# Kernel optimization log

Measured on AMD Instinct MI355X. Metric: run time of the kernel, lower is better.

Reference implementation:

```python
import jax, jax.numpy as jnp
import numpy as np

N_EMBED = 512  # scaling uses n_embed**-0.5 (as in the original, not head_dim)

def setup_inputs() -> dict:
    key = jax.random.key(0)
    k1, k2, k3 = jax.random.split(key, 3)
    B, T, HD = 4, 4096, 64
    return {
        "k": jax.random.normal(k1, (B, T, HD), dtype=jnp.float32),
        "q": jax.random.normal(k2, (B, T, HD), dtype=jnp.float32),
        "v": jax.random.normal(k3, (B, T, HD), dtype=jnp.float32),
    }

def reference(k, q, v):
    # wei = q @ k^T * n_embed^-0.5  -> [B, T, T]
    scale = N_EMBED ** (-0.5)
    wei = jnp.einsum("bqd,bkd->bqk", q, k) * scale
    T = q.shape[1]
    causal = jnp.tril(jnp.ones((T, T), dtype=bool))  # [T, T]
    wei = jnp.where(causal, wei, -jnp.inf)
    wei = jax.nn.softmax(wei, axis=-1)
    # dropout p=0.0 (identity)
    out = jnp.einsum("bqk,bkd->bqd", wei, v)
    return out
```

## Files before the change

### kernel.cpp

```cpp
#include <hip/hip_runtime.h>
#include <hip/hip_bf16.h>
#include <math.h>


typedef __attribute__((ext_vector_type(8))) __bf16 bf16x8;
typedef __attribute__((ext_vector_type(8))) short  short8;
typedef __attribute__((ext_vector_type(4))) float  f32x4;

#define TT 4096
#define DD 64
#define CH 6
#define NCHUNK_PB 187
#define NSLOT (NCHUNK_PB * 4)

static constexpr float SCALE_L2E = 0.06375871665087779f;

__device__ __forceinline__ ushort f2bf(float x) {
    return __builtin_bit_cast(ushort, (__bf16)x);
}
__device__ __forceinline__ float bf2f(ushort u) {
    return __builtin_bit_cast(float, ((unsigned)u) << 16);
}

__global__ __launch_bounds__(256, 1)
void prep(const float* __restrict__ K, const float* __restrict__ V,
          ushort* __restrict__ Kbf, ushort* __restrict__ Vtbf) {
    const int bx = blockIdx.x;
    const int b = bx & 3, kt = bx >> 2;
    const size_t tbase = (size_t)bx * 4096;
    const size_t gbase = (size_t)b * TT * DD + (size_t)(kt << 6) * DD;
    const int tid = threadIdx.x;

    {
        const int row = tid >> 2, q4 = tid & 3;
        const float* src = K + gbase + row * 64 + q4 * 16;
        ushort* dst = Kbf + tbase + row * 64;
        #pragma unroll
        for (int h = 0; h < 2; ++h) {
            f32x4 x = *(const f32x4*)(src + h * 8);
            f32x4 y = *(const f32x4*)(src + h * 8 + 4);
            union { ushort u[8]; short8 s; } pk;
            #pragma unroll
            for (int j = 0; j < 4; ++j) {
                pk.u[j]     = f2bf(x[j]);
                pk.u[j + 4] = f2bf(y[j]);
            }
            const int ch = (q4 * 2 + h) ^ (row & 7);
            *(short8*)(dst + ch * 8) = pk.s;
        }
    }
    {
        const int kp = tid & 31, dg = tid >> 5;
        const float* v0 = V + gbase + dg * 8 + kp * 2 * 64;
        f32x4 a0 = *(const f32x4*)(v0);
        f32x4 a1 = *(const f32x4*)(v0 + 4);
        f32x4 b0 = *(const f32x4*)(v0 + 64);
        f32x4 b1 = *(const f32x4*)(v0 + 68);
        #pragma unroll
        for (int j = 0; j < 8; ++j) {
            float xa = (j < 4) ? a0[j & 3] : a1[j & 3];
            float xb = (j < 4) ? b0[j & 3] : b1[j & 3];
            unsigned pk2 = (unsigned)f2bf(xa) | ((unsigned)f2bf(xb) << 16);
            const int dim = dg * 8 + j;
            const int off = dim * 64 + (((kp >> 2) ^ j) << 3) + ((kp * 2) & 7);
            *(unsigned*)(Vtbf + tbase + off) = pk2;
        }
    }
}

__global__ __launch_bounds__(256, 3)
void attn_part(const ushort* __restrict__ Kbf, const float* __restrict__ Q,
               const ushort* __restrict__ Vtbf,
               ushort* __restrict__ Opart, float* __restrict__ Lpart) {
    const int bx = blockIdx.x;
    const int b  = bx & 3;
    const int chunkid = bx >> 2;
    int s = 0, base = 0;
    for (;;) {
        const int nch = (s + 3) / 3;
        if (chunkid < base + nch) break;
        base += nch; ++s;
    }
    const int chunk = chunkid - base;

    const int tid = threadIdx.x;
    const int w = tid >> 6, lane = tid & 63;
    const int g = lane >> 4, c = lane & 15;
    const int qw0 = (s << 7) + (w << 5);

    __shared__ ushort lKV[2][2][4096];
    __shared__ ushort lP [4][1024];

    const int kt0 = chunk * CH;
    const int nst = min(kt0 + CH, 2 * (s + 1)) - kt0;
    const int seg0 = w * 1024;
    const int loff = lane * 8;

    {
        const size_t tb = (size_t)((kt0 << 2) | b) * 4096;
        #pragma unroll
        for (int p = 0; p < 2; ++p) {
            const int seg = seg0 + p * 512;
            __builtin_amdgcn_global_load_lds(
                (const __attribute__((address_space(1))) void*)(Kbf + tb + seg + loff),
                (__attribute__((address_space(3))) void*)&lKV[0][0][seg], 16, 0, 0);
            __builtin_amdgcn_global_load_lds(
                (const __attribute__((address_space(1))) void*)(Vtbf + tb + seg + loff),
                (__attribute__((address_space(3))) void*)&lKV[0][1][seg], 16, 0, 0);
        }
    }

    bf16x8 qf[2][2];
    #pragma unroll
    for (int m = 0; m < 2; ++m) {
        const float* qp = Q + (size_t)b * TT * DD
                        + (size_t)(qw0 + m * 16 + c) * DD + g * 8;
        #pragma unroll
        for (int ks = 0; ks < 2; ++ks) {
            f32x4 a = *(const f32x4*)(qp + ks * 32);
            f32x4 d = *(const f32x4*)(qp + ks * 32 + 4);
            bf16x8 t;
            #pragma unroll
            for (int j = 0; j < 4; ++j) {
                t[j]     = (__bf16)(a[j] * SCALE_L2E);
                t[j + 4] = (__bf16)(d[j] * SCALE_L2E);
            }
            qf[m][ks] = t;
        }
    }

    f32x4 acc[2][4];
    #pragma unroll
    for (int m = 0; m < 2; ++m)
        #pragma unroll
        for (int nt = 0; nt < 4; ++nt) acc[m][nt] = (f32x4){0.f, 0.f, 0.f, 0.f};
    float l_p[2][4] = {{0.f,0.f,0.f,0.f},{0.f,0.f,0.f,0.f}};

    for (int st = 0; st < nst; ++st) {
        const int kt = kt0 + st;
        const int kb = kt << 6;
        const int cur = st & 1;

        __syncthreads();

        if (st + 1 < nst) {
            const size_t tb = (size_t)(((kt + 1) << 2) | b) * 4096;
            #pragma unroll
            for (int p = 0; p < 2; ++p) {
                const int seg = seg0 + p * 512;
                __builtin_amdgcn_global_load_lds(
                    (const __attribute__((address_space(1))) void*)(Kbf + tb + seg + loff),
                    (__attribute__((address_space(3))) void*)&lKV[cur ^ 1][0][seg], 16, 0, 0);
                __builtin_amdgcn_global_load_lds(
                    (const __attribute__((address_space(1))) void*)(Vtbf + tb + seg + loff),
                    (__attribute__((address_space(3))) void*)&lKV[cur ^ 1][1][seg], 16, 0, 0);
            }
        }

        if (kb > qw0 + 31) continue;
        const bool act0 = (kb <= qw0 + 15);

        const ushort* lK  = lKV[cur][0];
        const ushort* lVt = lKV[cur][1];

        f32x4 S[2][4];
        #pragma unroll
        for (int nt = 0; nt < 4; ++nt) {
            const int row = nt * 16 + c;
            bf16x8 kf0 = __builtin_bit_cast(bf16x8,
                *(const short8*)&lK[row * 64 + (((0 * 4 + g) ^ (c & 7)) << 3)]);
            bf16x8 kf1 = __builtin_bit_cast(bf16x8,
                *(const short8*)&lK[row * 64 + (((1 * 4 + g) ^ (c & 7)) << 3)]);
            #pragma unroll
            for (int m = 0; m < 2; ++m) {
                if (m == 0 && !act0) continue;
                f32x4 sm = (f32x4){0.f, 0.f, 0.f, 0.f};
                sm = __builtin_amdgcn_mfma_f32_16x16x32_bf16(qf[m][0], kf0, sm, 0, 0, 0);
                sm = __builtin_amdgcn_mfma_f32_16x16x32_bf16(qf[m][1], kf1, sm, 0, 0, 0);
                S[m][nt] = sm;
            }
        }

        bf16x8 pf[2][2];
        #pragma unroll
        for (int m = 0; m < 2; ++m) {
            if (m == 0 && !act0) continue;
            const int qm0 = qw0 + m * 16;
            if (kb + 63 > qm0) {
                #pragma unroll
                for (int nt = 0; nt < 4; ++nt)
                    #pragma unroll
                    for (int r = 0; r < 4; ++r)
                        if (kb + nt * 16 + c > qm0 + g * 4 + r) S[m][nt][r] = -INFINITY;
            }
            ushort* myP = lP[w];
            #pragma unroll
            for (int nt = 0; nt < 4; ++nt)
                #pragma unroll
                for (int r = 0; r < 4; ++r) {
                    const float P = exp2f(S[m][nt][r]);
                    l_p[m][r] += P;
                    const int row = g * 4 + r;
                    const int col = nt * 16 + c;
                    myP[row * 64 + (((col >> 3) ^ (row & 7)) << 3) + (col & 7)] =
                        f2bf(P);
                }
            #pragma unroll
            for (int ks = 0; ks < 2; ++ks)
                pf[m][ks] = __builtin_bit_cast(bf16x8,
                    *(const short8*)&myP[c * 64 + (((ks * 4 + g) ^ (c & 7)) << 3)]);
        }

        #pragma unroll
        for (int ks = 0; ks < 2; ++ks)
            #pragma unroll
            for (int nt = 0; nt < 4; ++nt) {
                bf16x8 vf = __builtin_bit_cast(bf16x8,
                    *(const short8*)&lVt[(nt * 16 + c) * 64 + (((ks * 4 + g) ^ (c & 7)) << 3)]);
                #pragma unroll
                for (int m = 0; m < 2; ++m) {
                    if (m == 0 && !act0) continue;
                    acc[m][nt] = __builtin_amdgcn_mfma_f32_16x16x32_bf16(
                        pf[m][ks], vf, acc[m][nt], 0, 0, 0);
                }
            }
    }

    const int slot = bx;
    #pragma unroll
    for (int m = 0; m < 2; ++m) {
        #pragma unroll
        for (int r = 0; r < 4; ++r) {
            float l = l_p[m][r];
            #pragma unroll
            for (int off = 8; off >= 1; off >>= 1)
                l += __shfl_xor(l, off);
            l_p[m][r] = l;
        }
        union { ushort u[16]; short8 s8[2]; } pk;
        #pragma unroll
        for (int nt = 0; nt < 4; ++nt)
            #pragma unroll
            for (int r = 0; r < 4; ++r)
                pk.u[nt * 4 + r] = f2bf(acc[m][nt][r]);
        ushort* op = Opart + (size_t)slot * 8192 + (w * 2 + m) * 1024 + lane * 16;
        *(short8*)op       = pk.s8[0];
        *(short8*)(op + 8) = pk.s8[1];
        if (c == 0) {
            #pragma unroll
            for (int r = 0; r < 4; ++r)
                Lpart[(size_t)slot * 128 + (w * 2 + m) * 16 + g * 4 + r] = l_p[m][r];
        }
    }
}

__global__ __launch_bounds__(256, 1)
void attn_merge(const ushort* __restrict__ Opart, const float* __restrict__ Lpart,
                float* __restrict__ Out) {
    const int bx = blockIdx.x;
    const int b = bx & 3, s = (bx >> 2) & 31, w = bx >> 7;
    const int tid = threadIdx.x;
    const int m = tid >> 7, half = (tid >> 6) & 1, lane = tid & 63;
    const int g = lane >> 4;
    const int c = lane & 15;
    int base = 0;
    for (int t = 0; t < s; ++t) base += (t + 3) / 3;
    const int nch = (s + 3) / 3;

    float v[8];
    #pragma unroll
    for (int i = 0; i < 8; ++i) v[i] = 0.f;
    f32x4 lsum = (f32x4){0.f, 0.f, 0.f, 0.f};

    for (int ci = 0; ci < nch; ++ci) {
        const int slot = ((base + ci) << 2) | b;
        const ushort* op = Opart + (size_t)slot * 8192
                         + (w * 2 + m) * 1024 + lane * 16 + half * 8;
        short8 sv = *(const short8*)op;
        #pragma unroll
        for (int i = 0; i < 8; ++i) v[i] += bf2f((ushort)sv[i]);
        f32x4 lv = *(const f32x4*)(Lpart + (size_t)slot * 128 + (w * 2 + m) * 16 + g * 4);
        #pragma unroll
        for (int r = 0; r < 4; ++r) lsum[r] += lv[r];
    }

    f32x4 inv;
    #pragma unroll
    for (int r = 0; r < 4; ++r) inv[r] = 1.0f / lsum[r];

    const int qbase = (s << 7) + (w * 2 + m) * 16 + g * 4;
    float* dst = Out + (size_t)b * TT * DD;
    #pragma unroll
    for (int i = 0; i < 8; ++i) {
        const int nt = half * 2 + (i >> 2), r = i & 3;
        dst[(size_t)(qbase + r) * DD + nt * 16 + c] = v[i] * inv[r];
    }
}

__global__ __launch_bounds__(256, 1)
void attn_head(const float* __restrict__ K, const float* __restrict__ Q,
               const float* __restrict__ V, float* __restrict__ Out) {
    const int bx = blockIdx.x;
    const int b  = bx & 3;
    const int qt = bx >> 2;
    const int qbase = qt << 6;
    const int tid = threadIdx.x;
    const int w = tid >> 6, lane = tid & 63;
    const int g = lane >> 4, c = lane & 15;
    const int qr0 = qbase + (w << 4);

    __shared__ ushort lK [64 * 64];
    __shared__ ushort lVt[64 * 64];
    __shared__ ushort lP [4][16 * 64];

    const size_t bbase = (size_t)b * TT * DD;
    bf16x8 qf[2];
    {
        const float* qp = Q + bbase + (size_t)(qr0 + c) * DD + g * 8;
        #pragma unroll
        for (int ks = 0; ks < 2; ++ks) {
            f32x4 a = *(const f32x4*)(qp + ks * 32);
            f32x4 d = *(const f32x4*)(qp + ks * 32 + 4);
            bf16x8 t;
            #pragma unroll
            for (int j = 0; j < 4; ++j) {
                t[j]     = (__bf16)(a[j] * SCALE_L2E);
                t[j + 4] = (__bf16)(d[j] * SCALE_L2E);
            }
            qf[ks] = t;
        }
    }
    f32x4 acc[4];
    #pragma unroll
    for (int nt = 0; nt < 4; ++nt) acc[nt] = (f32x4){0.f, 0.f, 0.f, 0.f};
    float l_r[4] = {0.f, 0.f, 0.f, 0.f};
    const int e0  = w * 1024 + lane * 8;
    const int kch = ((lane & 7) ^ ((lane >> 3) & 7)) << 3;
    const int kp  = tid & 31, dg = tid >> 5;
    const int nkt = qt + 1;
    for (int kt = 0; kt < nkt; ++kt) {
        const int kb = kt << 6;
        __syncthreads();
        {
            const float* src = K + bbase + (size_t)kb * DD;
            #pragma unroll
            for (int p = 0; p < 2; ++p) {
                const int e = e0 + p * 512;
                f32x4 x = *(const f32x4*)(src + e);
                f32x4 y = *(const f32x4*)(src + e + 4);
                union { ushort u[8]; short8 s; } pk;
                #pragma unroll
                for (int j = 0; j < 4; ++j) {
                    pk.u[j]     = f2bf(x[j]);
                    pk.u[j + 4] = f2bf(y[j]);
                }
                *(short8*)&lK[(e >> 6) * 64 + kch] = pk.s;
            }
        }
        {
            const float* v0 = V + bbase + (size_t)kb * DD + dg * 8 + kp * 2 * 64;
            f32x4 a0 = *(const f32x4*)(v0);
            f32x4 a1 = *(const f32x4*)(v0 + 4);
            f32x4 b0 = *(const f32x4*)(v0 + 64);
            f32x4 b1 = *(const f32x4*)(v0 + 68);
            #pragma unroll
            for (int j = 0; j < 8; ++j) {
                float xa = (j < 4) ? a0[j & 3] : a1[j & 3];
                float xb = (j < 4) ? b0[j & 3] : b1[j & 3];
                unsigned pk2 = (unsigned)f2bf(xa) | ((unsigned)f2bf(xb) << 16);
                const int dim = dg * 8 + j;
                const int off = dim * 64 + (((kp >> 2) ^ j) << 3) + ((kp * 2) & 7);
                *(unsigned*)&lVt[off] = pk2;
            }
        }
        __syncthreads();
        if (kb <= qr0 + 15) {
            f32x4 S[4];
            #pragma unroll
            for (int nt = 0; nt < 4; ++nt) {
                const int row = nt * 16 + c;
                bf16x8 kf0 = __builtin_bit_cast(bf16x8,
                    *(const short8*)&lK[row * 64 + (((0 * 4 + g) ^ (c & 7)) << 3)]);
                bf16x8 kf1 = __builtin_bit_cast(bf16x8,
                    *(const short8*)&lK[row * 64 + (((1 * 4 + g) ^ (c & 7)) << 3)]);
                f32x4 sv = (f32x4){0.f, 0.f, 0.f, 0.f};
                sv = __builtin_amdgcn_mfma_f32_16x16x32_bf16(qf[0], kf0, sv, 0, 0, 0);
                sv = __builtin_amdgcn_mfma_f32_16x16x32_bf16(qf[1], kf1, sv, 0, 0, 0);
                S[nt] = sv;
            }
            if (kb + 63 > qr0) {
                #pragma unroll
                for (int nt = 0; nt < 4; ++nt)
                    #pragma unroll
                    for (int r = 0; r < 4; ++r)
                        if (kb + nt * 16 + c > qr0 + g * 4 + r) S[nt][r] = -INFINITY;
            }
            f32x4 P[4];
            #pragma unroll
            for (int nt = 0; nt < 4; ++nt)
                #pragma unroll
                for (int r = 0; r < 4; ++r)
                    P[nt][r] = exp2f(S[nt][r]);
            float ps[4];
            #pragma unroll
            for (int r = 0; r < 4; ++r)
                ps[r] = (P[0][r] + P[1][r]) + (P[2][r] + P[3][r]);
            #pragma unroll
            for (int off = 8; off >= 1; off >>= 1)
                #pragma unroll
                for (int r = 0; r < 4; ++r)
                    ps[r] += __shfl_xor(ps[r], off);
            #pragma unroll
            for (int r = 0; r < 4; ++r)
                l_r[r] += ps[r];
            ushort* myP = lP[w];
            #pragma unroll
            for (int nt = 0; nt < 4; ++nt)
                #pragma unroll
                for (int r = 0; r < 4; ++r) {
                    const int row = g * 4 + r;
                    const int col = nt * 16 + c;
                    myP[row * 64 + (((col >> 3) ^ (row & 7)) << 3) + (col & 7)] =
                        f2bf(P[nt][r]);
                }
            #pragma unroll
            for (int ks = 0; ks < 2; ++ks) {
                bf16x8 pf = __builtin_bit_cast(bf16x8,
                    *(const short8*)&myP[c * 64 + (((ks * 4 + g) ^ (c & 7)) << 3)]);
                #pragma unroll
                for (int nt = 0; nt < 4; ++nt) {
                    bf16x8 vf = __builtin_bit_cast(bf16x8,
                        *(const short8*)&lVt[(nt * 16 + c) * 64 + (((ks * 4 + g) ^ (c & 7)) << 3)]);
                    acc[nt] = __builtin_amdgcn_mfma_f32_16x16x32_bf16(pf, vf, acc[nt], 0, 0, 0);
                }
            }
        }
    }
    #pragma unroll
    for (int r = 0; r < 4; ++r) {
        const float inv = 1.0f / l_r[r];
        const size_t rowoff = bbase + (size_t)(qr0 + g * 4 + r) * DD;
        #pragma unroll
        for (int nt = 0; nt < 4; ++nt)
            Out[rowoff + nt * 16 + c] = acc[nt][r] * inv;
    }
}

extern "C" void kernel_launch(void* const* d_in, const int* in_sizes, int n_in,
                              void* d_out, int out_size, void* d_ws, size_t ws_size,
                              hipStream_t stream) {
    const float* k = (const float*)d_in[0];
    const float* q = (const float*)d_in[1];
    const float* v = (const float*)d_in[2];
    float* out = (float*)d_out;

    const size_t kv_elems = (size_t)4 * 64 * 4096;
    const size_t op_elems = (size_t)NSLOT * 8192;
    const size_t l_elems  = (size_t)NSLOT * 128;
    const size_t need = kv_elems * 2 * 2 + op_elems * 2 + l_elems * 4;
    if (ws_size >= need) {
        ushort* Kbf   = (ushort*)d_ws;
        ushort* Vtbf  = Kbf + kv_elems;
        ushort* Opart = Vtbf + kv_elems;
        float*  Lpart = (float*)(Opart + op_elems);
        hipLaunchKernelGGL(prep, dim3(256), dim3(256), 0, stream, k, v, Kbf, Vtbf);
        hipLaunchKernelGGL(attn_part, dim3(NSLOT), dim3(256), 0, stream,
                           Kbf, q, Vtbf, Opart, Lpart);
        hipLaunchKernelGGL(attn_merge, dim3(512), dim3(256), 0, stream,
                           Opart, Lpart, out);
    } else {
        hipLaunchKernelGGL(attn_head, dim3(256), dim3(256), 0, stream, k, q, v, out);
    }
}
```

Measured before the change: 98.26 us.

## Fuse K/V bf16 conversion into attention kernel and drop prep pass

Removes the separate prep kernel that converted K and V to swizzled bf16 tiles in a workspace. The attention kernel now loads fp32 K and V tiles into registers one step ahead, converts them, and writes the swizzled bf16 layout into shared memory itself before the barrier. This saves a kernel launch and the workspace write and read round trip. In exchange, every block reads twice as many bytes of K and V, redoes the conversion for tiles shared across blocks, and gives up asynchronous global-to-LDS loads in favour of a register-staged prefetch.

```diff
diff --git a/kernel.cpp b/kernel.cpp
--- a/kernel.cpp
+++ b/kernel.cpp
@@ -22,55 +22,9 @@
     return __builtin_bit_cast(float, ((unsigned)u) << 16);
 }
 
-__global__ __launch_bounds__(256, 1)
-void prep(const float* __restrict__ K, const float* __restrict__ V,
-          ushort* __restrict__ Kbf, ushort* __restrict__ Vtbf) {
-    const int bx = blockIdx.x;
-    const int b = bx & 3, kt = bx >> 2;
-    const size_t tbase = (size_t)bx * 4096;
-    const size_t gbase = (size_t)b * TT * DD + (size_t)(kt << 6) * DD;
-    const int tid = threadIdx.x;
-
-    {
-        const int row = tid >> 2, q4 = tid & 3;
-        const float* src = K + gbase + row * 64 + q4 * 16;
-        ushort* dst = Kbf + tbase + row * 64;
-        #pragma unroll
-        for (int h = 0; h < 2; ++h) {
-            f32x4 x = *(const f32x4*)(src + h * 8);
-            f32x4 y = *(const f32x4*)(src + h * 8 + 4);
-            union { ushort u[8]; short8 s; } pk;
-            #pragma unroll
-            for (int j = 0; j < 4; ++j) {
-                pk.u[j]     = f2bf(x[j]);
-                pk.u[j + 4] = f2bf(y[j]);
-            }
-            const int ch = (q4 * 2 + h) ^ (row & 7);
-            *(short8*)(dst + ch * 8) = pk.s;
-        }
-    }
-    {
-        const int kp = tid & 31, dg = tid >> 5;
-        const float* v0 = V + gbase + dg * 8 + kp * 2 * 64;
-        f32x4 a0 = *(const f32x4*)(v0);
-        f32x4 a1 = *(const f32x4*)(v0 + 4);
-        f32x4 b0 = *(const f32x4*)(v0 + 64);
-        f32x4 b1 = *(const f32x4*)(v0 + 68);
-        #pragma unroll
-        for (int j = 0; j < 8; ++j) {
-            float xa = (j < 4) ? a0[j & 3] : a1[j & 3];
-            float xb = (j < 4) ? b0[j & 3] : b1[j & 3];
-            unsigned pk2 = (unsigned)f2bf(xa) | ((unsigned)f2bf(xb) << 16);
-            const int dim = dg * 8 + j;
-            const int off = dim * 64 + (((kp >> 2) ^ j) << 3) + ((kp * 2) & 7);
-            *(unsigned*)(Vtbf + tbase + off) = pk2;
-        }
-    }
-}
-
 __global__ __launch_bounds__(256, 3)
-void attn_part(const ushort* __restrict__ Kbf, const float* __restrict__ Q,
-               const ushort* __restrict__ Vtbf,
+void attn_part(const float* __restrict__ K, const float* __restrict__ Q,
+               const float* __restrict__ V,
                ushort* __restrict__ Opart, float* __restrict__ Lpart) {
     const int bx = blockIdx.x;
     const int b  = bx & 3;
@@ -93,28 +47,35 @@
 
     const int kt0 = chunk * CH;
     const int nst = min(kt0 + CH, 2 * (s + 1)) - kt0;
-    const int seg0 = w * 1024;
-    const int loff = lane * 8;
-
-    {
-        const size_t tb = (size_t)((kt0 << 2) | b) * 4096;
-        #pragma unroll
-        for (int p = 0; p < 2; ++p) {
-            const int seg = seg0 + p * 512;
-            __builtin_amdgcn_global_load_lds(
-                (const __attribute__((address_space(1))) void*)(Kbf + tb + seg + loff),
-                (__attribute__((address_space(3))) void*)&lKV[0][0][seg], 16, 0, 0);
-            __builtin_amdgcn_global_load_lds(
-                (const __attribute__((address_space(1))) void*)(Vtbf + tb + seg + loff),
-                (__attribute__((address_space(3))) void*)&lKV[0][1][seg], 16, 0, 0);
-        }
-    }
+
+    const size_t bbase = (size_t)b * TT * DD;
+
+    const int e0  = w * 1024 + lane * 8;
+    const int kch = ((lane & 7) ^ ((lane >> 3) & 7)) << 3;
+    const int kp  = tid & 31, dg = tid >> 5;
+
+    f32x4 kx0, ky0, kx1, ky1;
+    f32x4 va0, va1, vb0, vb1;
+
+    auto load_raw = [&](int kt) {
+        const float* src = K + bbase + (size_t)(kt << 6) * DD;
+        kx0 = *(const f32x4*)(src + e0);
+        ky0 = *(const f32x4*)(src + e0 + 4);
+        kx1 = *(const f32x4*)(src + e0 + 512);
+        ky1 = *(const f32x4*)(src + e0 + 516);
+        const float* v0 = V + bbase + (size_t)(kt << 6) * DD + dg * 8 + kp * 2 * 64;
+        va0 = *(const f32x4*)(v0);
+        va1 = *(const f32x4*)(v0 + 4);
+        vb0 = *(const f32x4*)(v0 + 64);
+        vb1 = *(const f32x4*)(v0 + 68);
+    };
+
+    load_raw(kt0);
 
     bf16x8 qf[2][2];
     #pragma unroll
     for (int m = 0; m < 2; ++m) {
-        const float* qp = Q + (size_t)b * TT * DD
-                        + (size_t)(qw0 + m * 16 + c) * DD + g * 8;
+        const float* qp = Q + bbase + (size_t)(qw0 + m * 16 + c) * DD + g * 8;
         #pragma unroll
         for (int ks = 0; ks < 2; ++ks) {
             f32x4 a = *(const f32x4*)(qp + ks * 32);
@@ -141,21 +102,38 @@
         const int kb = kt << 6;
         const int cur = st & 1;
 
+        {
+            ushort* dK = lKV[cur][0];
+            #pragma unroll
+            for (int p = 0; p < 2; ++p) {
+                const f32x4 x = p ? kx1 : kx0;
+                const f32x4 y = p ? ky1 : ky0;
+                union { ushort u[8]; short8 s8; } pk;
+                #pragma unroll
+                for (int j = 0; j < 4; ++j) {
+                    pk.u[j]     = f2bf(x[j]);
+                    pk.u[j + 4] = f2bf(y[j]);
+                }
+                const int e = e0 + p * 512;
+                *(short8*)&dK[(e >> 6) * 64 + kch] = pk.s8;
+            }
+        }
+        {
+            ushort* dV = lKV[cur][1];
+            #pragma unroll
+            for (int j = 0; j < 8; ++j) {
+                const float xa = (j < 4) ? va0[j & 3] : va1[j & 3];
+                const float xb = (j < 4) ? vb0[j & 3] : vb1[j & 3];
+                const unsigned pk2 = (unsigned)f2bf(xa) | ((unsigned)f2bf(xb) << 16);
+                const int dim = dg * 8 + j;
+                const int off = dim * 64 + (((kp >> 2) ^ j) << 3) + ((kp * 2) & 7);
+                *(unsigned*)&dV[off] = pk2;
+            }
+        }
+
+        if (st + 1 < nst) load_raw(kt + 1);
+
         __syncthreads();
-
-        if (st + 1 < nst) {
-            const size_t tb = (size_t)(((kt + 1) << 2) | b) * 4096;
-            #pragma unroll
-            for (int p = 0; p < 2; ++p) {
-                const int seg = seg0 + p * 512;
-                __builtin_amdgcn_global_load_lds(
-                    (const __attribute__((address_space(1))) void*)(Kbf + tb + seg + loff),
-                    (__attribute__((address_space(3))) void*)&lKV[cur ^ 1][0][seg], 16, 0, 0);
-                __builtin_amdgcn_global_load_lds(
-                    (const __attribute__((address_space(1))) void*)(Vtbf + tb + seg + loff),
-                    (__attribute__((address_space(3))) void*)&lKV[cur ^ 1][1][seg], 16, 0, 0);
-            }
-        }
 
         if (kb > qw0 + 31) continue;
         const bool act0 = (kb <= qw0 + 15);
@@ -454,18 +432,14 @@
     const float* v = (const float*)d_in[2];
     float* out = (float*)d_out;
 
-    const size_t kv_elems = (size_t)4 * 64 * 4096;
     const size_t op_elems = (size_t)NSLOT * 8192;
     const size_t l_elems  = (size_t)NSLOT * 128;
-    const size_t need = kv_elems * 2 * 2 + op_elems * 2 + l_elems * 4;
+    const size_t need = op_elems * 2 + l_elems * 4;
     if (ws_size >= need) {
-        ushort* Kbf   = (ushort*)d_ws;
-        ushort* Vtbf  = Kbf + kv_elems;
-        ushort* Opart = Vtbf + kv_elems;
+        ushort* Opart = (ushort*)d_ws;
         float*  Lpart = (float*)(Opart + op_elems);
-        hipLaunchKernelGGL(prep, dim3(256), dim3(256), 0, stream, k, v, Kbf, Vtbf);
         hipLaunchKernelGGL(attn_part, dim3(NSLOT), dim3(256), 0, stream,
-                           Kbf, q, Vtbf, Opart, Lpart);
+                           k, q, v, Opart, Lpart);
         hipLaunchKernelGGL(attn_merge, dim3(512), dim3(256), 0, stream,
                            Opart, Lpart, out);
     } else {
```

Result: slower. 110.5 us (+12.5%).
